# Kernel tuning notes

Hardware: AMD Instinct MI355X
Metric: run time of the kernel (lower is better)

## Reference

```python
import jax, jax.numpy as jnp
import numpy as np
from jax import lax


def ternary_quant(w):
    # Layer-wise ternary quantization: alpha = mean(|w|), threshold = 0.001*alpha
    alpha = lax.stop_gradient(jnp.mean(jnp.abs(w)))
    thr = 0.001 * alpha
    q = jnp.where(w > thr, 1.0, jnp.where(w < -thr, -1.0, 0.0))
    return alpha * q


def setup_inputs() -> dict:
    key = jax.random.key(0)
    k1, k2, k3, k4, k5 = jax.random.split(key, 5)
    B, C, H, W = 32, 384, 64, 64
    fan_in = C * 3 * 3
    bound = 1.0 / np.sqrt(fan_in)  # torch Conv2d default init scale
    return {
        "x": jax.random.normal(k1, (B, C, H, W), dtype=jnp.float32),
        "weight": jax.random.uniform(k2, (C, C, 3, 3), dtype=jnp.float32, minval=-bound, maxval=bound),
        "bias": jax.random.uniform(k3, (C,), dtype=jnp.float32, minval=-bound, maxval=bound),
        "time_emb": jax.random.normal(k4, (B, 512), dtype=jnp.float32),
        "y": jax.random.randint(k5, (B,), 0, 1000, dtype=jnp.int64),
    }


def reference(x, weight, bias, time_emb, y):
    # time_emb and y are accepted but unused, matching Downsample.forward
    qw = ternary_quant(weight)
    out = lax.conv_general_dilated(
        x, qw,
        window_strides=(2, 2),
        padding=((1, 1), (1, 1)),
        dimension_numbers=("NCHW", "OIHW", "NCHW"),
    )
    return out + bias[None, :, None, None]
```

## Files before the change

### kernel.cpp

```cpp
#include <hip/hip_runtime.h>
#include <hip/hip_bf16.h>


#define CIN   384
#define HIN   64
#define WIN   64
#define OHW   32
#define KDIM  3456
#define NWELT 1327104
#define MDIM  32768
#define NT    54

using bf16 = __hip_bfloat16;
typedef __attribute__((ext_vector_type(8))) short short8;
typedef __attribute__((ext_vector_type(4))) float floatx4;
typedef __attribute__((ext_vector_type(2))) unsigned short ushort2v;

#define AS1 __attribute__((address_space(1)))
#define AS3 __attribute__((address_space(3)))
#define DMA16(g, l) __builtin_amdgcn_global_load_lds((const AS1 void*)(g), (AS3 void*)(l), 16, 0, 0)

#define EDGE(N) do { \
    asm volatile("s_waitcnt vmcnt(" #N ")" ::: "memory"); \
    __builtin_amdgcn_s_barrier(); \
    __builtin_amdgcn_sched_barrier(0); \
} while (0)

#define NPART  62
#define ZG_F   16
#define XN_OFF 256
#define WQ_OFF (256 + 100663296)

__global__ void absum_part(const float* __restrict__ w, float* __restrict__ ws) {
    const float4* w4 = (const float4*)w;
    float s = 0.f;
    for (int i = blockIdx.x * 256 + threadIdx.x; i < NWELT / 4; i += NPART * 256) {
        float4 v = w4[i];
        s += fabsf(v.x) + fabsf(v.y) + fabsf(v.z) + fabsf(v.w);
    }
    for (int off = 32; off; off >>= 1) s += __shfl_down(s, off, 64);
    __shared__ float red[4];
    if ((threadIdx.x & 63) == 0) red[threadIdx.x >> 6] = s;
    __syncthreads();
    if (threadIdx.x == 0) ws[2 + blockIdx.x] = red[0] + red[1] + red[2] + red[3];
}

__global__ void absum_final(float* __restrict__ ws) {
    if (threadIdx.x == 0) {
        float s = 0.f;
        for (int i = 0; i < NPART; ++i) s += ws[2 + i];
        float alpha = s * (1.0f / NWELT);
        ws[0] = alpha;
        ws[1] = 1e-3f * alpha;
        ws[ZG_F + 0] = 0.f; ws[ZG_F + 1] = 0.f;
        ws[ZG_F + 2] = 0.f; ws[ZG_F + 3] = 0.f;
    }
}

__global__ void quant_kernel(const float* __restrict__ w, const float* __restrict__ ws,
                             bf16* __restrict__ wq) {
    int j = blockIdx.x * 256 + threadIdx.x;
    if (j >= NWELT) return;
    float thr = ws[1];
    int o = j / KDIM;
    int rmd = j - o * KDIM;
    int khkw = rmd / 384;
    int c = rmd - khkw * 384;
    float v = w[((o * 384 + c) * 9) + khkw];
    float q = (v > thr) ? 1.f : ((v < -thr) ? -1.f : 0.f);
    wq[j] = __float2bfloat16(q);
}

__global__ void nhwc_kernel(const float* __restrict__ x, bf16* __restrict__ xn) {
    int nh = blockIdx.x;
    int n = nh >> 6, h = nh & 63;
    int c0 = blockIdx.y * 64;
    __shared__ bf16 tile[64][66];
    const float* src = x + ((n * CIN + c0) * HIN + h) * WIN;
    for (int i = 0; i < 4; ++i) {
        int s = threadIdx.x + i * 256;
        int cl = s >> 4, w4 = (s & 15) * 4;
        float4 v = *(const float4*)(src + cl * 4096 + w4);
        bf16 t0[2], t1[2];
        t0[0] = __float2bfloat16(v.x); t0[1] = __float2bfloat16(v.y);
        t1[0] = __float2bfloat16(v.z); t1[1] = __float2bfloat16(v.w);
        *(ushort2v*)&tile[cl][w4]     = *(ushort2v*)t0;
        *(ushort2v*)&tile[cl][w4 + 2] = *(ushort2v*)t1;
    }
    __syncthreads();
    bf16* dst = xn + ((size_t)(n * HIN + h) * WIN) * CIN + c0;
    for (int i = 0; i < 2; ++i) {
        int q = threadIdx.x + i * 256;
        int wc = q >> 3, c8 = (q & 7) * 8;
        bf16 tmp[8];
        #pragma unroll
        for (int j = 0; j < 8; ++j) tmp[j] = tile[c8 + j][wc];
        *(short8*)(dst + (size_t)wc * CIN + c8) = *(short8*)tmp;
    }
}

#define BM  128

__global__ __launch_bounds__(512, 2) void conv_gemm(const bf16* __restrict__ xn,
                                                    const bf16* __restrict__ wq,
                                                    const float* __restrict__ ws,
                                                    const float* __restrict__ bias,
                                                    float* __restrict__ out,
                                                    const bf16* __restrict__ zg) {
    __shared__ __align__(16) bf16 lW[2][384 * 64];
    __shared__ __align__(16) bf16 lX[2][128 * 64];
    const int m_base = blockIdx.x * BM;
    const int tid = threadIdx.x;
    const int lane = tid & 63;
    const int wv = tid >> 6;
    const int io = wv & 3;
    const int im = wv >> 2;
    const int g = (lane & 7) ^ (lane >> 3);

    const bf16* pw[2][3];
    int wLoff[2][3];
    #pragma unroll
    for (int h = 0; h < 2; ++h)
        #pragma unroll
        for (int j = 0; j < 3; ++j) {
            int rr = h * 192 + wv * 24 + j * 8;
            pw[h][j] = wq + (size_t)(rr + (lane >> 3)) * KDIM + g * 8;
            wLoff[h][j] = rr * 64;
        }
    const bf16* pxn[2];
    int oh2[2], ow2[2], xLoff[2];
    #pragma unroll
    for (int h = 0; h < 2; ++h) {
        int rr = h * 64 + wv * 8;
        int m = m_base + rr + (lane >> 3);
        int n = m >> 10, oh = (m >> 5) & 31, ow = m & 31;
        pxn[h] = xn + (size_t)n * (HIN * WIN * CIN) + g * 8;
        oh2[h] = 2 * oh - 1;
        ow2[h] = 2 * ow - 1;
        xLoff[h] = rr * 64;
    }

    const int l15 = lane & 15, quad = lane >> 4, l7 = lane & 7;
    const int octA = (quad ^ l7) * 8;
    const int octB = ((4 + quad) ^ l7) * 8;
    int aoff[2][3], boff[2][2];
    #pragma unroll
    for (int h = 0; h < 2; ++h)
        #pragma unroll
        for (int fo = 0; fo < 3; ++fo)
            aoff[h][fo] = (h * 192 + io * 48 + fo * 16 + l15) * 64;
    #pragma unroll
    for (int h = 0; h < 2; ++h)
        #pragma unroll
        for (int fm = 0; fm < 2; ++fm)
            boff[h][fm] = (h * 64 + im * 32 + fm * 16 + l15) * 64;

    floatx4 acc[6][4];
    #pragma unroll
    for (int i = 0; i < 6; ++i)
        #pragma unroll
        for (int j = 0; j < 4; ++j)
            acc[i][j] = (floatx4){0.f, 0.f, 0.f, 0.f};

    {
        #pragma unroll
        for (int j = 0; j < 3; ++j) DMA16(pw[0][j], &lW[0][wLoff[0][j]]);
        {
            int ih = oh2[0], iw = ow2[0];
            const bf16* p = (ih >= 0 && iw >= 0) ? pxn[0] + (ih * WIN + iw) * CIN : zg;
            DMA16(p, &lX[0][xLoff[0]]);
        }
        {
            int ih = oh2[1], iw = ow2[1];
            const bf16* p = (ih >= 0 && iw >= 0) ? pxn[1] + (ih * WIN + iw) * CIN : zg;
            DMA16(p, &lX[0][xLoff[1]]);
        }
        #pragma unroll
        for (int j = 0; j < 3; ++j) DMA16(pw[1][j], &lW[0][wLoff[1][j]]);
        EDGE(4);
    }

    short8 af[2][3], bfl[2][2], bfh[2][2];

    for (int t = 0; t < NT - 1; ++t) {
        bf16* lWc = lW[t & 1];
        bf16* lXc = lX[t & 1];
        bf16* lWn = lW[(t & 1) ^ 1];
        bf16* lXn = lX[(t & 1) ^ 1];
        const int s = t + 1;
        const int kk = s / 6, cs = s - kk * 6;
        const int kh = kk / 3, kw = kk - kh * 3;
        const int ws64 = s * 64;
        const bf16* pxs[2];
        #pragma unroll
        for (int h = 0; h < 2; ++h) {
            int ih = oh2[h] + kh, iw = ow2[h] + kw;
            pxs[h] = (ih >= 0 && iw >= 0) ? pxn[h] + (ih * WIN + iw) * CIN + cs * 64 : zg;
        }

        #pragma unroll
        for (int fo = 0; fo < 3; ++fo) {
            af[0][fo] = *(const short8*)(lWc + aoff[0][fo] + octA);
            af[1][fo] = *(const short8*)(lWc + aoff[0][fo] + octB);
        }
        #pragma unroll
        for (int fm = 0; fm < 2; ++fm) {
            bfl[0][fm] = *(const short8*)(lXc + boff[0][fm] + octA);
            bfl[1][fm] = *(const short8*)(lXc + boff[0][fm] + octB);
        }
        #pragma unroll
        for (int j = 0; j < 3; ++j) DMA16(pw[0][j] + ws64, lWn + wLoff[0][j]);
        EDGE(6);
        __builtin_amdgcn_s_setprio(1);
        #pragma unroll
        for (int ks = 0; ks < 2; ++ks)
            #pragma unroll
            for (int fo = 0; fo < 3; ++fo)
                #pragma unroll
                for (int fm = 0; fm < 2; ++fm)
                    acc[fo][fm] = __builtin_amdgcn_mfma_f32_16x16x32_bf16(
                        af[ks][fo], bfl[ks][fm], acc[fo][fm], 0, 0, 0);
        __builtin_amdgcn_s_setprio(0);

        #pragma unroll
        for (int fm = 0; fm < 2; ++fm) {
            bfh[0][fm] = *(const short8*)(lXc + boff[1][fm] + octA);
            bfh[1][fm] = *(const short8*)(lXc + boff[1][fm] + octB);
        }
        DMA16(pxs[0], lXn + xLoff[0]);
        EDGE(4);
        __builtin_amdgcn_s_setprio(1);
        #pragma unroll
        for (int ks = 0; ks < 2; ++ks)
            #pragma unroll
            for (int fo = 0; fo < 3; ++fo)
                #pragma unroll
                for (int fm = 0; fm < 2; ++fm)
                    acc[fo][2 + fm] = __builtin_amdgcn_mfma_f32_16x16x32_bf16(
                        af[ks][fo], bfh[ks][fm], acc[fo][2 + fm], 0, 0, 0);
        __builtin_amdgcn_s_setprio(0);

        #pragma unroll
        for (int fo = 0; fo < 3; ++fo) {
            af[0][fo] = *(const short8*)(lWc + aoff[1][fo] + octA);
            af[1][fo] = *(const short8*)(lWc + aoff[1][fo] + octB);
        }
        DMA16(pxs[1], lXn + xLoff[1]);
        __builtin_amdgcn_s_setprio(1);
        #pragma unroll
        for (int ks = 0; ks < 2; ++ks)
            #pragma unroll
            for (int fo = 0; fo < 3; ++fo)
                #pragma unroll
                for (int fm = 0; fm < 2; ++fm)
                    acc[3 + fo][2 + fm] = __builtin_amdgcn_mfma_f32_16x16x32_bf16(
                        af[ks][fo], bfh[ks][fm], acc[3 + fo][2 + fm], 0, 0, 0);
        __builtin_amdgcn_s_setprio(0);

        #pragma unroll
        for (int j = 0; j < 3; ++j) DMA16(pw[1][j] + ws64, lWn + wLoff[1][j]);
        EDGE(4);
        __builtin_amdgcn_s_setprio(1);
        #pragma unroll
        for (int ks = 0; ks < 2; ++ks)
            #pragma unroll
            for (int fo = 0; fo < 3; ++fo)
                #pragma unroll
                for (int fm = 0; fm < 2; ++fm)
                    acc[3 + fo][fm] = __builtin_amdgcn_mfma_f32_16x16x32_bf16(
                        af[ks][fo], bfl[ks][fm], acc[3 + fo][fm], 0, 0, 0);
        __builtin_amdgcn_s_setprio(0);
    }

    {
        bf16* lWc = lW[1];
        bf16* lXc = lX[1];
        #pragma unroll
        for (int fo = 0; fo < 3; ++fo) {
            af[0][fo] = *(const short8*)(lWc + aoff[0][fo] + octA);
            af[1][fo] = *(const short8*)(lWc + aoff[0][fo] + octB);
        }
        #pragma unroll
        for (int fm = 0; fm < 2; ++fm) {
            bfl[0][fm] = *(const short8*)(lXc + boff[0][fm] + octA);
            bfl[1][fm] = *(const short8*)(lXc + boff[0][fm] + octB);
        }
        EDGE(3);
        __builtin_amdgcn_s_setprio(1);
        #pragma unroll
        for (int ks = 0; ks < 2; ++ks)
            #pragma unroll
            for (int fo = 0; fo < 3; ++fo)
                #pragma unroll
                for (int fm = 0; fm < 2; ++fm)
                    acc[fo][fm] = __builtin_amdgcn_mfma_f32_16x16x32_bf16(
                        af[ks][fo], bfl[ks][fm], acc[fo][fm], 0, 0, 0);
        __builtin_amdgcn_s_setprio(0);
        #pragma unroll
        for (int fm = 0; fm < 2; ++fm) {
            bfh[0][fm] = *(const short8*)(lXc + boff[1][fm] + octA);
            bfh[1][fm] = *(const short8*)(lXc + boff[1][fm] + octB);
        }
        EDGE(0);
        __builtin_amdgcn_s_setprio(1);
        #pragma unroll
        for (int ks = 0; ks < 2; ++ks)
            #pragma unroll
            for (int fo = 0; fo < 3; ++fo)
                #pragma unroll
                for (int fm = 0; fm < 2; ++fm)
                    acc[fo][2 + fm] = __builtin_amdgcn_mfma_f32_16x16x32_bf16(
                        af[ks][fo], bfh[ks][fm], acc[fo][2 + fm], 0, 0, 0);
        __builtin_amdgcn_s_setprio(0);
        #pragma unroll
        for (int fo = 0; fo < 3; ++fo) {
            af[0][fo] = *(const short8*)(lWc + aoff[1][fo] + octA);
            af[1][fo] = *(const short8*)(lWc + aoff[1][fo] + octB);
        }
        __builtin_amdgcn_s_setprio(1);
        #pragma unroll
        for (int ks = 0; ks < 2; ++ks)
            #pragma unroll
            for (int fo = 0; fo < 3; ++fo)
                #pragma unroll
                for (int fm = 0; fm < 2; ++fm)
                    acc[3 + fo][2 + fm] = __builtin_amdgcn_mfma_f32_16x16x32_bf16(
                        af[ks][fo], bfh[ks][fm], acc[3 + fo][2 + fm], 0, 0, 0);
        __builtin_amdgcn_s_setprio(0);
        __builtin_amdgcn_s_setprio(1);
        #pragma unroll
        for (int ks = 0; ks < 2; ++ks)
            #pragma unroll
            for (int fo = 0; fo < 3; ++fo)
                #pragma unroll
                for (int fm = 0; fm < 2; ++fm)
                    acc[3 + fo][fm] = __builtin_amdgcn_mfma_f32_16x16x32_bf16(
                        af[ks][fo], bfl[ks][fm], acc[3 + fo][fm], 0, 0, 0);
        __builtin_amdgcn_s_setprio(0);
    }

    float alpha = ws[0];
    #pragma unroll
    for (int i = 0; i < 6; ++i) {
        int o0 = (i / 3) * 192 + io * 48 + (i % 3) * 16 + quad * 4;
        #pragma unroll
        for (int j = 0; j < 4; ++j) {
            int m = m_base + (j >> 1) * 64 + im * 32 + (j & 1) * 16 + l15;
            int n = m >> 10, ohh = (m >> 5) & 31, oww = m & 31;
            #pragma unroll
            for (int r = 0; r < 4; ++r) {
                int o = o0 + r;
                out[((n * 384 + o) * OHW + ohh) * OHW + oww] = alpha * acc[i][j][r] + bias[o];
            }
        }
    }
}

extern "C" void kernel_launch(void* const* d_in, const int* in_sizes, int n_in,
                              void* d_out, int out_size, void* d_ws, size_t ws_size,
                              hipStream_t stream) {
    (void)in_sizes; (void)n_in; (void)out_size; (void)ws_size;
    const float* x    = (const float*)d_in[0];
    const float* w    = (const float*)d_in[1];
    const float* bias = (const float*)d_in[2];
    float* out = (float*)d_out;
    float* wsf = (float*)d_ws;
    bf16* xn = (bf16*)((char*)d_ws + XN_OFF);
    bf16* wq = (bf16*)((char*)d_ws + WQ_OFF);
    const bf16* zg = (const bf16*)(wsf + ZG_F);

    absum_part<<<NPART, 256, 0, stream>>>(w, wsf);
    absum_final<<<1, 64, 0, stream>>>(wsf);
    quant_kernel<<<(NWELT + 255) / 256, 256, 0, stream>>>(w, wsf, wq);
    nhwc_kernel<<<dim3(2048, 6), 256, 0, stream>>>(x, xn);
    conv_gemm<<<dim3(MDIM / BM, 1), 512, 0, stream>>>(xn, wq, wsf, bias, out, zg);
}
```

Measured before the change: 426.3 us.

## Fuse NCHW-to-NHWC bf16 conversion into the conv GEMM's input tile loading

```diff
diff --git a/kernel.cpp b/kernel.cpp
--- a/kernel.cpp
+++ b/kernel.cpp
@@ -14,21 +14,25 @@
 using bf16 = __hip_bfloat16;
 typedef __attribute__((ext_vector_type(8))) short short8;
 typedef __attribute__((ext_vector_type(4))) float floatx4;
-typedef __attribute__((ext_vector_type(2))) unsigned short ushort2v;
 
 #define AS1 __attribute__((address_space(1)))
 #define AS3 __attribute__((address_space(3)))
 #define DMA16(g, l) __builtin_amdgcn_global_load_lds((const AS1 void*)(g), (AS3 void*)(l), 16, 0, 0)
 
-#define EDGE(N) do { \
+#define EDGE_V(N) do { \
     asm volatile("s_waitcnt vmcnt(" #N ")" ::: "memory"); \
     __builtin_amdgcn_s_barrier(); \
     __builtin_amdgcn_sched_barrier(0); \
 } while (0)
+#define EDGE_VL(N) do { \
+    asm volatile("s_waitcnt vmcnt(" #N ")" ::: "memory"); \
+    asm volatile("s_waitcnt lgkmcnt(0)" ::: "memory"); \
+    __builtin_amdgcn_s_barrier(); \
+    __builtin_amdgcn_sched_barrier(0); \
+} while (0)
 
 #define NPART  62
 #define ZG_F   16
-#define XN_OFF 256
 #define WQ_OFF (256 + 100663296)
 
 __global__ void absum_part(const float* __restrict__ w, float* __restrict__ ws) {
@@ -71,42 +75,19 @@
     wq[j] = __float2bfloat16(q);
 }
 
-__global__ void nhwc_kernel(const float* __restrict__ x, bf16* __restrict__ xn) {
-    int nh = blockIdx.x;
-    int n = nh >> 6, h = nh & 63;
-    int c0 = blockIdx.y * 64;
-    __shared__ bf16 tile[64][66];
-    const float* src = x + ((n * CIN + c0) * HIN + h) * WIN;
-    for (int i = 0; i < 4; ++i) {
-        int s = threadIdx.x + i * 256;
-        int cl = s >> 4, w4 = (s & 15) * 4;
-        float4 v = *(const float4*)(src + cl * 4096 + w4);
-        bf16 t0[2], t1[2];
-        t0[0] = __float2bfloat16(v.x); t0[1] = __float2bfloat16(v.y);
-        t1[0] = __float2bfloat16(v.z); t1[1] = __float2bfloat16(v.w);
-        *(ushort2v*)&tile[cl][w4]     = *(ushort2v*)t0;
-        *(ushort2v*)&tile[cl][w4 + 2] = *(ushort2v*)t1;
-    }
-    __syncthreads();
-    bf16* dst = xn + ((size_t)(n * HIN + h) * WIN) * CIN + c0;
-    for (int i = 0; i < 2; ++i) {
-        int q = threadIdx.x + i * 256;
-        int wc = q >> 3, c8 = (q & 7) * 8;
-        bf16 tmp[8];
-        #pragma unroll
-        for (int j = 0; j < 8; ++j) tmp[j] = tile[c8 + j][wc];
-        *(short8*)(dst + (size_t)wc * CIN + c8) = *(short8*)tmp;
-    }
-}
-
 #define BM  128
 
-__global__ __launch_bounds__(512, 2) void conv_gemm(const bf16* __restrict__ xn,
+#define CVT(f) ((short)__builtin_bit_cast(unsigned short, __float2bfloat16(f)))
+
+__device__ __forceinline__ void xput(bf16* lXn, int m, int co, short8 v) {
+    *(short8*)((char*)lXn + m * 128 + ((co ^ (m & 7)) << 4)) = v;
+}
+
+__global__ __launch_bounds__(512, 2) void conv_gemm(const float* __restrict__ x,
                                                     const bf16* __restrict__ wq,
                                                     const float* __restrict__ ws,
                                                     const float* __restrict__ bias,
-                                                    float* __restrict__ out,
-                                                    const bf16* __restrict__ zg) {
+                                                    float* __restrict__ out) {
     __shared__ __align__(16) bf16 lW[2][384 * 64];
     __shared__ __align__(16) bf16 lX[2][128 * 64];
     const int m_base = blockIdx.x * BM;
@@ -117,6 +98,9 @@
     const int im = wv >> 2;
     const int g = (lane & 7) ^ (lane >> 3);
 
+    const int n = m_base >> 10;
+    const int oh0 = (m_base >> 5) & 31;
+
     const bf16* pw[2][3];
     int wLoff[2][3];
     #pragma unroll
@@ -127,18 +111,12 @@
             pw[h][j] = wq + (size_t)(rr + (lane >> 3)) * KDIM + g * 8;
             wLoff[h][j] = rr * 64;
         }
-    const bf16* pxn[2];
-    int oh2[2], ow2[2], xLoff[2];
-    #pragma unroll
-    for (int h = 0; h < 2; ++h) {
-        int rr = h * 64 + wv * 8;
-        int m = m_base + rr + (lane >> 3);
-        int n = m >> 10, oh = (m >> 5) & 31, ow = m & 31;
-        pxn[h] = xn + (size_t)n * (HIN * WIN * CIN) + g * 8;
-        oh2[h] = 2 * oh - 1;
-        ow2[h] = 2 * ow - 1;
-        xLoff[h] = rr * 64;
-    }
+
+    const int co  = tid & 7;
+    const int owp = (tid >> 3) & 15;
+    const int ohx = tid >> 7;
+    const int ohb = 2 * (oh0 + ohx) - 1;
+    const float* xrow0 = x + ((size_t)(n * CIN + co * 8) * HIN) * WIN + owp * 4;
 
     const int l15 = lane & 15, quad = lane >> 4, l7 = lane & 7;
     const int octA = (quad ^ l7) * 8;
@@ -162,22 +140,37 @@
         for (int j = 0; j < 4; ++j)
             acc[i][j] = (floatx4){0.f, 0.f, 0.f, 0.f};
 
+    short8 zv;
+    #pragma unroll
+    for (int i = 0; i < 8; ++i) zv[i] = 0;
+
     {
+        float4 xr[8];
+        const int ihv = ohb;
+        if (ihv >= 0) {
+            const float* xb = xrow0 + (size_t)ihv * WIN;
+            #pragma unroll
+            for (int i = 0; i < 8; ++i) xr[i] = *(const float4*)(xb + i * 4096);
+        } else {
+            #pragma unroll
+            for (int i = 0; i < 8; ++i) xr[i] = make_float4(0.f, 0.f, 0.f, 0.f);
+        }
         #pragma unroll
         for (int j = 0; j < 3; ++j) DMA16(pw[0][j], &lW[0][wLoff[0][j]]);
-        {
-            int ih = oh2[0], iw = ow2[0];
-            const bf16* p = (ih >= 0 && iw >= 0) ? pxn[0] + (ih * WIN + iw) * CIN : zg;
-            DMA16(p, &lX[0][xLoff[0]]);
-        }
-        {
-            int ih = oh2[1], iw = ow2[1];
-            const bf16* p = (ih >= 0 && iw >= 0) ? pxn[1] + (ih * WIN + iw) * CIN : zg;
-            DMA16(p, &lX[0][xLoff[1]]);
-        }
         #pragma unroll
         for (int j = 0; j < 3; ++j) DMA16(pw[1][j], &lW[0][wLoff[1][j]]);
-        EDGE(4);
+        short8 v0, v1;
+        if (ihv >= 0) {
+            #pragma unroll
+            for (int i = 0; i < 8; ++i) { v0[i] = CVT(xr[i].y); v1[i] = CVT(xr[i].w); }
+        } else { v0 = zv; v1 = zv; }
+        xput(lX[0], ohx * 32 + owp * 2 + 1, co, v0);
+        if (owp < 15) xput(lX[0], ohx * 32 + owp * 2 + 2, co, v1);
+        if (owp == 0) xput(lX[0], ohx * 32, co, zv);
+        asm volatile("s_waitcnt lgkmcnt(0)" ::: "memory");
+        asm volatile("s_waitcnt vmcnt(3)" ::: "memory");
+        __builtin_amdgcn_s_barrier();
+        __builtin_amdgcn_sched_barrier(0);
     }
 
     short8 af[2][3], bfl[2][2], bfh[2][2];
@@ -188,15 +181,12 @@
         bf16* lWn = lW[(t & 1) ^ 1];
         bf16* lXn = lX[(t & 1) ^ 1];
         const int s = t + 1;
-        const int kk = s / 6, cs = s - kk * 6;
-        const int kh = kk / 3, kw = kk - kh * 3;
-        const int ws64 = s * 64;
-        const bf16* pxs[2];
-        #pragma unroll
-        for (int h = 0; h < 2; ++h) {
-            int ih = oh2[h] + kh, iw = ow2[h] + kw;
-            pxs[h] = (ih >= 0 && iw >= 0) ? pxn[h] + (ih * WIN + iw) * CIN + cs * 64 : zg;
-        }
+        const int cc_s = s / 9;
+        const int khkw_s = s - cc_s * 9;
+        const int kh_s = khkw_s / 3;
+        const int kw_s = khkw_s - kh_s * 3;
+        const int koff = khkw_s * 384 + cc_s * 64;
+        const int ihv = ohb + kh_s;
 
         #pragma unroll
         for (int fo = 0; fo < 3; ++fo) {
@@ -208,9 +198,17 @@
             bfl[0][fm] = *(const short8*)(lXc + boff[0][fm] + octA);
             bfl[1][fm] = *(const short8*)(lXc + boff[0][fm] + octB);
         }
-        #pragma unroll
-        for (int j = 0; j < 3; ++j) DMA16(pw[0][j] + ws64, lWn + wLoff[0][j]);
-        EDGE(6);
+        float4 xr[8];
+        if (ihv >= 0) {
+            const float* xb = xrow0 + ((size_t)cc_s * 64 * HIN + ihv) * WIN;
+            #pragma unroll
+            for (int i = 0; i < 8; ++i) xr[i] = *(const float4*)(xb + i * 4096);
+        } else {
+            #pragma unroll
+            for (int i = 0; i < 8; ++i) xr[i] = make_float4(0.f, 0.f, 0.f, 0.f);
+        }
+        #pragma unroll
+        for (int j = 0; j < 3; ++j) DMA16(pw[0][j] + koff, lWn + wLoff[0][j]);
         __builtin_amdgcn_s_setprio(1);
         #pragma unroll
         for (int ks = 0; ks < 2; ++ks)
@@ -227,8 +225,7 @@
             bfh[0][fm] = *(const short8*)(lXc + boff[1][fm] + octA);
             bfh[1][fm] = *(const short8*)(lXc + boff[1][fm] + octB);
         }
-        DMA16(pxs[0], lXn + xLoff[0]);
-        EDGE(4);
+        EDGE_V(11);
         __builtin_amdgcn_s_setprio(1);
         #pragma unroll
         for (int ks = 0; ks < 2; ++ks)
@@ -245,7 +242,6 @@
             af[0][fo] = *(const short8*)(lWc + aoff[1][fo] + octA);
             af[1][fo] = *(const short8*)(lWc + aoff[1][fo] + octB);
         }
-        DMA16(pxs[1], lXn + xLoff[1]);
         __builtin_amdgcn_s_setprio(1);
         #pragma unroll
         for (int ks = 0; ks < 2; ++ks)
@@ -256,10 +252,30 @@
                     acc[3 + fo][2 + fm] = __builtin_amdgcn_mfma_f32_16x16x32_bf16(
                         af[ks][fo], bfh[ks][fm], acc[3 + fo][2 + fm], 0, 0, 0);
         __builtin_amdgcn_s_setprio(0);
-
-        #pragma unroll
-        for (int j = 0; j < 3; ++j) DMA16(pw[1][j] + ws64, lWn + wLoff[1][j]);
-        EDGE(4);
+        {
+            short8 v0, v1;
+            if (ihv >= 0) {
+                if (kw_s == 1) {
+                    #pragma unroll
+                    for (int i = 0; i < 8; ++i) { v0[i] = CVT(xr[i].x); v1[i] = CVT(xr[i].z); }
+                } else {
+                    #pragma unroll
+                    for (int i = 0; i < 8; ++i) { v0[i] = CVT(xr[i].y); v1[i] = CVT(xr[i].w); }
+                }
+            } else { v0 = zv; v1 = zv; }
+            if (kw_s == 0) {
+                xput(lXn, ohx * 32 + owp * 2 + 1, co, v0);
+                if (owp < 15) xput(lXn, ohx * 32 + owp * 2 + 2, co, v1);
+                if (owp == 0) xput(lXn, ohx * 32, co, zv);
+            } else {
+                xput(lXn, ohx * 32 + owp * 2, co, v0);
+                xput(lXn, ohx * 32 + owp * 2 + 1, co, v1);
+            }
+        }
+
+        #pragma unroll
+        for (int j = 0; j < 3; ++j) DMA16(pw[1][j] + koff, lWn + wLoff[1][j]);
+        EDGE_VL(3);
         __builtin_amdgcn_s_setprio(1);
         #pragma unroll
         for (int ks = 0; ks < 2; ++ks)
@@ -285,7 +301,6 @@
             bfl[0][fm] = *(const short8*)(lXc + boff[0][fm] + octA);
             bfl[1][fm] = *(const short8*)(lXc + boff[0][fm] + octB);
         }
-        EDGE(3);
         __builtin_amdgcn_s_setprio(1);
         #pragma unroll
         for (int ks = 0; ks < 2; ++ks)
@@ -301,7 +316,7 @@
             bfh[0][fm] = *(const short8*)(lXc + boff[1][fm] + octA);
             bfh[1][fm] = *(const short8*)(lXc + boff[1][fm] + octB);
         }
-        EDGE(0);
+        EDGE_V(0);
         __builtin_amdgcn_s_setprio(1);
         #pragma unroll
         for (int ks = 0; ks < 2; ++ks)
@@ -346,11 +361,11 @@
         #pragma unroll
         for (int j = 0; j < 4; ++j) {
             int m = m_base + (j >> 1) * 64 + im * 32 + (j & 1) * 16 + l15;
-            int n = m >> 10, ohh = (m >> 5) & 31, oww = m & 31;
+            int nn = m >> 10, ohh = (m >> 5) & 31, oww = m & 31;
             #pragma unroll
             for (int r = 0; r < 4; ++r) {
                 int o = o0 + r;
-                out[((n * 384 + o) * OHW + ohh) * OHW + oww] = alpha * acc[i][j][r] + bias[o];
+                out[((nn * 384 + o) * OHW + ohh) * OHW + oww] = alpha * acc[i][j][r] + bias[o];
             }
         }
     }
@@ -365,13 +380,10 @@
     const float* bias = (const float*)d_in[2];
     float* out = (float*)d_out;
     float* wsf = (float*)d_ws;
-    bf16* xn = (bf16*)((char*)d_ws + XN_OFF);
     bf16* wq = (bf16*)((char*)d_ws + WQ_OFF);
-    const bf16* zg = (const bf16*)(wsf + ZG_F);
 
     absum_part<<<NPART, 256, 0, stream>>>(w, wsf);
     absum_final<<<1, 64, 0, stream>>>(wsf);
     quant_kernel<<<(NWELT + 255) / 256, 256, 0, stream>>>(w, wsf, wq);
-    nhwc_kernel<<<dim3(2048, 6), 256, 0, stream>>>(x, xn);
-    conv_gemm<<<dim3(MDIM / BM, 1), 512, 0, stream>>>(xn, wq, wsf, bias, out, zg);
-}
+    conv_gemm<<<dim3(MDIM / BM, 1), 512, 0, stream>>>(x, wq, wsf, bias, out);
+}
```

After: 436.0 us. 1.02x slower.

## Triple-buffer activation tiles and prefetch two K-steps ahead in conv GEMM

Applied to the files above, without the earlier changes.

```diff
diff --git a/kernel.cpp b/kernel.cpp
--- a/kernel.cpp
+++ b/kernel.cpp
@@ -20,10 +20,29 @@
 #define AS3 __attribute__((address_space(3)))
 #define DMA16(g, l) __builtin_amdgcn_global_load_lds((const AS1 void*)(g), (AS3 void*)(l), 16, 0, 0)
 
-#define EDGE(N) do { \
+#define EDGE_V(N) do { \
     asm volatile("s_waitcnt vmcnt(" #N ")" ::: "memory"); \
     __builtin_amdgcn_s_barrier(); \
     __builtin_amdgcn_sched_barrier(0); \
+} while (0)
+#define EDGE_VL(N) do { \
+    asm volatile("s_waitcnt vmcnt(" #N ")" ::: "memory"); \
+    asm volatile("s_waitcnt lgkmcnt(0)" ::: "memory"); \
+    __builtin_amdgcn_s_barrier(); \
+    __builtin_amdgcn_sched_barrier(0); \
+} while (0)
+
+#define MFMA_Q(ACCR, ACCC, BF) do { \
+    __builtin_amdgcn_s_setprio(1); \
+    _Pragma("unroll") \
+    for (int ks = 0; ks < 2; ++ks) \
+        _Pragma("unroll") \
+        for (int fo = 0; fo < 3; ++fo) \
+            _Pragma("unroll") \
+            for (int fm = 0; fm < 2; ++fm) \
+                acc[(ACCR) + fo][(ACCC) + fm] = __builtin_amdgcn_mfma_f32_16x16x32_bf16( \
+                    af[ks][fo], BF[ks][fm], acc[(ACCR) + fo][(ACCC) + fm], 0, 0, 0); \
+    __builtin_amdgcn_s_setprio(0); \
 } while (0)
 
 #define NPART  62
@@ -108,7 +127,7 @@
                                                     float* __restrict__ out,
                                                     const bf16* __restrict__ zg) {
     __shared__ __align__(16) bf16 lW[2][384 * 64];
-    __shared__ __align__(16) bf16 lX[2][128 * 64];
+    __shared__ __align__(16) bf16 lX[3][128 * 64];
     const int m_base = blockIdx.x * BM;
     const int tid = threadIdx.x;
     const int lane = tid & 63;
@@ -127,6 +146,7 @@
             pw[h][j] = wq + (size_t)(rr + (lane >> 3)) * KDIM + g * 8;
             wLoff[h][j] = rr * 64;
         }
+
     const bf16* pxn[2];
     int oh2[2], ow2[2], xLoff[2];
     #pragma unroll
@@ -164,39 +184,35 @@
 
     {
         #pragma unroll
-        for (int j = 0; j < 3; ++j) DMA16(pw[0][j], &lW[0][wLoff[0][j]]);
-        {
-            int ih = oh2[0], iw = ow2[0];
-            const bf16* p = (ih >= 0 && iw >= 0) ? pxn[0] + (ih * WIN + iw) * CIN : zg;
-            DMA16(p, &lX[0][xLoff[0]]);
-        }
-        {
-            int ih = oh2[1], iw = ow2[1];
-            const bf16* p = (ih >= 0 && iw >= 0) ? pxn[1] + (ih * WIN + iw) * CIN : zg;
-            DMA16(p, &lX[0][xLoff[1]]);
-        }
-        #pragma unroll
-        for (int j = 0; j < 3; ++j) DMA16(pw[1][j], &lW[0][wLoff[1][j]]);
-        EDGE(4);
+        for (int h = 0; h < 2; ++h) {
+            int ih = oh2[h], iw = ow2[h];
+            const bf16* p = (ih >= 0 && iw >= 0) ? pxn[h] + (ih * WIN + iw) * CIN : zg;
+            DMA16(p, &lX[0][xLoff[h]]);
+        }
+        #pragma unroll
+        for (int h = 0; h < 2; ++h)
+            #pragma unroll
+            for (int j = 0; j < 3; ++j) DMA16(pw[h][j], &lW[0][wLoff[h][j]]);
+        #pragma unroll
+        for (int h = 0; h < 2; ++h) {
+            int ih = oh2[h], iw = ow2[h];
+            const bf16* p = (ih >= 0 && iw >= 0) ? pxn[h] + (ih * WIN + iw) * CIN + 64 : zg;
+            DMA16(p, &lX[1][xLoff[h]]);
+        }
+        EDGE_V(2);
     }
 
     short8 af[2][3], bfl[2][2], bfh[2][2];
 
     for (int t = 0; t < NT - 1; ++t) {
         bf16* lWc = lW[t & 1];
-        bf16* lXc = lX[t & 1];
-        bf16* lWn = lW[(t & 1) ^ 1];
-        bf16* lXn = lX[(t & 1) ^ 1];
-        const int s = t + 1;
-        const int kk = s / 6, cs = s - kk * 6;
-        const int kh = kk / 3, kw = kk - kh * 3;
-        const int ws64 = s * 64;
-        const bf16* pxs[2];
-        #pragma unroll
-        for (int h = 0; h < 2; ++h) {
-            int ih = oh2[h] + kh, iw = ow2[h] + kw;
-            pxs[h] = (ih >= 0 && iw >= 0) ? pxn[h] + (ih * WIN + iw) * CIN + cs * 64 : zg;
-        }
+        const int x_cur = t % 3;
+        bf16* lWn = lW[(t + 1) & 1];
+        bf16* lXn2 = lX[(t + 2) % 3];
+        const int kW = (t + 1) * 64;
+        const int s2 = t + 2;
+        const int khkw2 = s2 / 6, cc2 = s2 - khkw2 * 6;
+        const int kh2 = khkw2 / 3, kw2 = khkw2 - kh2 * 3;
 
         #pragma unroll
         for (int fo = 0; fo < 3; ++fo) {
@@ -205,138 +221,68 @@
         }
         #pragma unroll
         for (int fm = 0; fm < 2; ++fm) {
+            bfl[0][fm] = *(const short8*)(lX[x_cur] + boff[0][fm] + octA);
+            bfl[1][fm] = *(const short8*)(lX[x_cur] + boff[0][fm] + octB);
+        }
+        #pragma unroll
+        for (int h = 0; h < 2; ++h)
+            #pragma unroll
+            for (int j = 0; j < 3; ++j) DMA16(pw[h][j] + kW, lWn + wLoff[h][j]);
+        MFMA_Q(0, 0, bfl);
+
+        #pragma unroll
+        for (int fm = 0; fm < 2; ++fm) {
+            bfh[0][fm] = *(const short8*)(lX[x_cur] + boff[1][fm] + octA);
+            bfh[1][fm] = *(const short8*)(lX[x_cur] + boff[1][fm] + octB);
+        }
+        #pragma unroll
+        for (int h = 0; h < 2; ++h) {
+            int ih = oh2[h] + kh2, iw = ow2[h] + kw2;
+            bool valid = (ih >= 0) & (iw >= 0) & (s2 < NT);
+            const bf16* p = valid ? pxn[h] + (ih * WIN + iw) * CIN + cc2 * 64 : zg;
+            DMA16(p, lXn2 + xLoff[h]);
+        }
+        EDGE_V(8);
+        MFMA_Q(0, 2, bfh);
+
+        #pragma unroll
+        for (int fo = 0; fo < 3; ++fo) {
+            af[0][fo] = *(const short8*)(lWc + aoff[1][fo] + octA);
+            af[1][fo] = *(const short8*)(lWc + aoff[1][fo] + octB);
+        }
+        MFMA_Q(3, 2, bfh);
+
+        EDGE_VL(2);
+        MFMA_Q(3, 0, bfl);
+    }
+
+    {
+        bf16* lWc = lW[1];
+        bf16* lXc = lX[53 % 3];
+        #pragma unroll
+        for (int fo = 0; fo < 3; ++fo) {
+            af[0][fo] = *(const short8*)(lWc + aoff[0][fo] + octA);
+            af[1][fo] = *(const short8*)(lWc + aoff[0][fo] + octB);
+        }
+        #pragma unroll
+        for (int fm = 0; fm < 2; ++fm) {
             bfl[0][fm] = *(const short8*)(lXc + boff[0][fm] + octA);
             bfl[1][fm] = *(const short8*)(lXc + boff[0][fm] + octB);
         }
-        #pragma unroll
-        for (int j = 0; j < 3; ++j) DMA16(pw[0][j] + ws64, lWn + wLoff[0][j]);
-        EDGE(6);
-        __builtin_amdgcn_s_setprio(1);
-        #pragma unroll
-        for (int ks = 0; ks < 2; ++ks)
-            #pragma unroll
-            for (int fo = 0; fo < 3; ++fo)
-                #pragma unroll
-                for (int fm = 0; fm < 2; ++fm)
-                    acc[fo][fm] = __builtin_amdgcn_mfma_f32_16x16x32_bf16(
-                        af[ks][fo], bfl[ks][fm], acc[fo][fm], 0, 0, 0);
-        __builtin_amdgcn_s_setprio(0);
-
+        MFMA_Q(0, 0, bfl);
         #pragma unroll
         for (int fm = 0; fm < 2; ++fm) {
             bfh[0][fm] = *(const short8*)(lXc + boff[1][fm] + octA);
             bfh[1][fm] = *(const short8*)(lXc + boff[1][fm] + octB);
         }
-        DMA16(pxs[0], lXn + xLoff[0]);
-        EDGE(4);
-        __builtin_amdgcn_s_setprio(1);
-        #pragma unroll
-        for (int ks = 0; ks < 2; ++ks)
-            #pragma unroll
-            for (int fo = 0; fo < 3; ++fo)
-                #pragma unroll
-                for (int fm = 0; fm < 2; ++fm)
-                    acc[fo][2 + fm] = __builtin_amdgcn_mfma_f32_16x16x32_bf16(
-                        af[ks][fo], bfh[ks][fm], acc[fo][2 + fm], 0, 0, 0);
-        __builtin_amdgcn_s_setprio(0);
-
+        MFMA_Q(0, 2, bfh);
         #pragma unroll
         for (int fo = 0; fo < 3; ++fo) {
             af[0][fo] = *(const short8*)(lWc + aoff[1][fo] + octA);
             af[1][fo] = *(const short8*)(lWc + aoff[1][fo] + octB);
         }
-        DMA16(pxs[1], lXn + xLoff[1]);
-        __builtin_amdgcn_s_setprio(1);
-        #pragma unroll
-        for (int ks = 0; ks < 2; ++ks)
-            #pragma unroll
-            for (int fo = 0; fo < 3; ++fo)
-                #pragma unroll
-                for (int fm = 0; fm < 2; ++fm)
-                    acc[3 + fo][2 + fm] = __builtin_amdgcn_mfma_f32_16x16x32_bf16(
-                        af[ks][fo], bfh[ks][fm], acc[3 + fo][2 + fm], 0, 0, 0);
-        __builtin_amdgcn_s_setprio(0);
-
-        #pragma unroll
-        for (int j = 0; j < 3; ++j) DMA16(pw[1][j] + ws64, lWn + wLoff[1][j]);
-        EDGE(4);
-        __builtin_amdgcn_s_setprio(1);
-        #pragma unroll
-        for (int ks = 0; ks < 2; ++ks)
-            #pragma unroll
-            for (int fo = 0; fo < 3; ++fo)
-                #pragma unroll
-                for (int fm = 0; fm < 2; ++fm)
-                    acc[3 + fo][fm] = __builtin_amdgcn_mfma_f32_16x16x32_bf16(
-                        af[ks][fo], bfl[ks][fm], acc[3 + fo][fm], 0, 0, 0);
-        __builtin_amdgcn_s_setprio(0);
-    }
-
-    {
-        bf16* lWc = lW[1];
-        bf16* lXc = lX[1];
-        #pragma unroll
-        for (int fo = 0; fo < 3; ++fo) {
-            af[0][fo] = *(const short8*)(lWc + aoff[0][fo] + octA);
-            af[1][fo] = *(const short8*)(lWc + aoff[0][fo] + octB);
-        }
-        #pragma unroll
-        for (int fm = 0; fm < 2; ++fm) {
-            bfl[0][fm] = *(const short8*)(lXc + boff[0][fm] + octA);
-            bfl[1][fm] = *(const short8*)(lXc + boff[0][fm] + octB);
-        }
-        EDGE(3);
-        __builtin_amdgcn_s_setprio(1);
-        #pragma unroll
-        for (int ks = 0; ks < 2; ++ks)
-            #pragma unroll
-            for (int fo = 0; fo < 3; ++fo)
-                #pragma unroll
-                for (int fm = 0; fm < 2; ++fm)
-                    acc[fo][fm] = __builtin_amdgcn_mfma_f32_16x16x32_bf16(
-                        af[ks][fo], bfl[ks][fm], acc[fo][fm], 0, 0, 0);
-        __builtin_amdgcn_s_setprio(0);
-        #pragma unroll
-        for (int fm = 0; fm < 2; ++fm) {
-            bfh[0][fm] = *(const short8*)(lXc + boff[1][fm] + octA);
-            bfh[1][fm] = *(const short8*)(lXc + boff[1][fm] + octB);
-        }
-        EDGE(0);
-        __builtin_amdgcn_s_setprio(1);
-        #pragma unroll
-        for (int ks = 0; ks < 2; ++ks)
-            #pragma unroll
-            for (int fo = 0; fo < 3; ++fo)
-                #pragma unroll
-                for (int fm = 0; fm < 2; ++fm)
-                    acc[fo][2 + fm] = __builtin_amdgcn_mfma_f32_16x16x32_bf16(
-                        af[ks][fo], bfh[ks][fm], acc[fo][2 + fm], 0, 0, 0);
-        __builtin_amdgcn_s_setprio(0);
-        #pragma unroll
-        for (int fo = 0; fo < 3; ++fo) {
-            af[0][fo] = *(const short8*)(lWc + aoff[1][fo] + octA);
-            af[1][fo] = *(const short8*)(lWc + aoff[1][fo] + octB);
-        }
-        __builtin_amdgcn_s_setprio(1);
-        #pragma unroll
-        for (int ks = 0; ks < 2; ++ks)
-            #pragma unroll
-            for (int fo = 0; fo < 3; ++fo)
-                #pragma unroll
-                for (int fm = 0; fm < 2; ++fm)
-                    acc[3 + fo][2 + fm] = __builtin_amdgcn_mfma_f32_16x16x32_bf16(
-                        af[ks][fo], bfh[ks][fm], acc[3 + fo][2 + fm], 0, 0, 0);
-        __builtin_amdgcn_s_setprio(0);
-        __builtin_amdgcn_s_setprio(1);
-        #pragma unroll
-        for (int ks = 0; ks < 2; ++ks)
-            #pragma unroll
-            for (int fo = 0; fo < 3; ++fo)
-                #pragma unroll
-                for (int fm = 0; fm < 2; ++fm)
-                    acc[3 + fo][fm] = __builtin_amdgcn_mfma_f32_16x16x32_bf16(
-                        af[ks][fo], bfl[ks][fm], acc[3 + fo][fm], 0, 0, 0);
-        __builtin_amdgcn_s_setprio(0);
+        MFMA_Q(3, 2, bfh);
+        MFMA_Q(3, 0, bfl);
     }
 
     float alpha = ws[0];
@@ -346,11 +292,11 @@
         #pragma unroll
         for (int j = 0; j < 4; ++j) {
             int m = m_base + (j >> 1) * 64 + im * 32 + (j & 1) * 16 + l15;
-            int n = m >> 10, ohh = (m >> 5) & 31, oww = m & 31;
+            int nn = m >> 10, ohh = (m >> 5) & 31, oww = m & 31;
             #pragma unroll
             for (int r = 0; r < 4; ++r) {
                 int o = o0 + r;
-                out[((n * 384 + o) * OHW + ohh) * OHW + oww] = alpha * acc[i][j][r] + bias[o];
+                out[((nn * 384 + o) * OHW + ohh) * OHW + oww] = alpha * acc[i][j][r] + bias[o];
             }
         }
     }
```

Result: slower. 437.5 us (+2.6%).

## Triple-buffer input tiles and prefetch activations two K-steps ahead

Applied to the files above, without the earlier changes.

```diff
diff --git a/kernel.cpp b/kernel.cpp
--- a/kernel.cpp
+++ b/kernel.cpp
@@ -20,7 +20,7 @@
 #define AS3 __attribute__((address_space(3)))
 #define DMA16(g, l) __builtin_amdgcn_global_load_lds((const AS1 void*)(g), (AS3 void*)(l), 16, 0, 0)
 
-#define EDGE(N) do { \
+#define EDGE_V(N) do { \
     asm volatile("s_waitcnt vmcnt(" #N ")" ::: "memory"); \
     __builtin_amdgcn_s_barrier(); \
     __builtin_amdgcn_sched_barrier(0); \
@@ -108,7 +108,7 @@
                                                     float* __restrict__ out,
                                                     const bf16* __restrict__ zg) {
     __shared__ __align__(16) bf16 lW[2][384 * 64];
-    __shared__ __align__(16) bf16 lX[2][128 * 64];
+    __shared__ __align__(16) bf16 lX[3][128 * 64];
     const int m_base = blockIdx.x * BM;
     const int tid = threadIdx.x;
     const int lane = tid & 63;
@@ -164,38 +164,41 @@
 
     {
         #pragma unroll
-        for (int j = 0; j < 3; ++j) DMA16(pw[0][j], &lW[0][wLoff[0][j]]);
-        {
-            int ih = oh2[0], iw = ow2[0];
-            const bf16* p = (ih >= 0 && iw >= 0) ? pxn[0] + (ih * WIN + iw) * CIN : zg;
-            DMA16(p, &lX[0][xLoff[0]]);
-        }
-        {
-            int ih = oh2[1], iw = ow2[1];
-            const bf16* p = (ih >= 0 && iw >= 0) ? pxn[1] + (ih * WIN + iw) * CIN : zg;
-            DMA16(p, &lX[0][xLoff[1]]);
-        }
-        #pragma unroll
-        for (int j = 0; j < 3; ++j) DMA16(pw[1][j], &lW[0][wLoff[1][j]]);
-        EDGE(4);
+        for (int h = 0; h < 2; ++h) {
+            int ih = oh2[h], iw = ow2[h];
+            const bf16* p = (ih >= 0 && iw >= 0) ? pxn[h] + (ih * WIN + iw) * CIN : zg;
+            DMA16(p, &lX[0][xLoff[h]]);
+        }
+        #pragma unroll
+        for (int h = 0; h < 2; ++h)
+            #pragma unroll
+            for (int j = 0; j < 3; ++j) DMA16(pw[h][j], &lW[0][wLoff[h][j]]);
+        #pragma unroll
+        for (int h = 0; h < 2; ++h) {
+            int ih = oh2[h], iw = ow2[h];
+            const bf16* p = (ih >= 0 && iw >= 0) ? pxn[h] + (ih * WIN + iw) * CIN + 64 : zg;
+            DMA16(p, &lX[1][xLoff[h]]);
+        }
+        EDGE_V(2);
     }
 
     short8 af[2][3], bfl[2][2], bfh[2][2];
 
     for (int t = 0; t < NT - 1; ++t) {
-        bf16* lWc = lW[t & 1];
-        bf16* lXc = lX[t & 1];
-        bf16* lWn = lW[(t & 1) ^ 1];
-        bf16* lXn = lX[(t & 1) ^ 1];
-        const int s = t + 1;
-        const int kk = s / 6, cs = s - kk * 6;
-        const int kh = kk / 3, kw = kk - kh * 3;
-        const int ws64 = s * 64;
+        const bf16* lWc = lW[t & 1];
+        const bf16* lXc = lX[t % 3];
+        bf16* lWn = lW[(t + 1) & 1];
+        bf16* lXn2 = lX[(t + 2) % 3];
+        const int kW = (t + 1) * 64;
+        const int s2 = t + 2;
+        const int kk2 = s2 / 6, cs2 = s2 - kk2 * 6;
+        const int kh2 = kk2 / 3, kw2 = kk2 - kh2 * 3;
         const bf16* pxs[2];
         #pragma unroll
         for (int h = 0; h < 2; ++h) {
-            int ih = oh2[h] + kh, iw = ow2[h] + kw;
-            pxs[h] = (ih >= 0 && iw >= 0) ? pxn[h] + (ih * WIN + iw) * CIN + cs * 64 : zg;
+            int ih = oh2[h] + kh2, iw = ow2[h] + kw2;
+            bool valid = (ih >= 0) & (iw >= 0) & (s2 < NT);
+            pxs[h] = valid ? pxn[h] + (ih * WIN + iw) * CIN + cs2 * 64 : zg;
         }
 
         #pragma unroll
@@ -209,8 +212,8 @@
             bfl[1][fm] = *(const short8*)(lXc + boff[0][fm] + octB);
         }
         #pragma unroll
-        for (int j = 0; j < 3; ++j) DMA16(pw[0][j] + ws64, lWn + wLoff[0][j]);
-        EDGE(6);
+        for (int j = 0; j < 3; ++j) DMA16(pw[0][j] + kW, lWn + wLoff[0][j]);
+        EDGE_V(5);
         __builtin_amdgcn_s_setprio(1);
         #pragma unroll
         for (int ks = 0; ks < 2; ++ks)
@@ -227,8 +230,9 @@
             bfh[0][fm] = *(const short8*)(lXc + boff[1][fm] + octA);
             bfh[1][fm] = *(const short8*)(lXc + boff[1][fm] + octB);
         }
-        DMA16(pxs[0], lXn + xLoff[0]);
-        EDGE(4);
+        #pragma unroll
+        for (int j = 0; j < 3; ++j) DMA16(pw[1][j] + kW, lWn + wLoff[1][j]);
+        EDGE_V(8);
         __builtin_amdgcn_s_setprio(1);
         #pragma unroll
         for (int ks = 0; ks < 2; ++ks)
@@ -245,7 +249,8 @@
             af[0][fo] = *(const short8*)(lWc + aoff[1][fo] + octA);
             af[1][fo] = *(const short8*)(lWc + aoff[1][fo] + octB);
         }
-        DMA16(pxs[1], lXn + xLoff[1]);
+        DMA16(pxs[0], lXn2 + xLoff[0]);
+        EDGE_V(9);
         __builtin_amdgcn_s_setprio(1);
         #pragma unroll
         for (int ks = 0; ks < 2; ++ks)
@@ -257,9 +262,8 @@
                         af[ks][fo], bfh[ks][fm], acc[3 + fo][2 + fm], 0, 0, 0);
         __builtin_amdgcn_s_setprio(0);
 
-        #pragma unroll
-        for (int j = 0; j < 3; ++j) DMA16(pw[1][j] + ws64, lWn + wLoff[1][j]);
-        EDGE(4);
+        DMA16(pxs[1], lXn2 + xLoff[1]);
+        EDGE_V(2);
         __builtin_amdgcn_s_setprio(1);
         #pragma unroll
         for (int ks = 0; ks < 2; ++ks)
@@ -273,8 +277,8 @@
     }
 
     {
-        bf16* lWc = lW[1];
-        bf16* lXc = lX[1];
+        const bf16* lWc = lW[1];
+        const bf16* lXc = lX[53 % 3];
         #pragma unroll
         for (int fo = 0; fo < 3; ++fo) {
             af[0][fo] = *(const short8*)(lWc + aoff[0][fo] + octA);
@@ -285,7 +289,6 @@
             bfl[0][fm] = *(const short8*)(lXc + boff[0][fm] + octA);
             bfl[1][fm] = *(const short8*)(lXc + boff[0][fm] + octB);
         }
-        EDGE(3);
         __builtin_amdgcn_s_setprio(1);
         #pragma unroll
         for (int ks = 0; ks < 2; ++ks)
@@ -301,7 +304,6 @@
             bfh[0][fm] = *(const short8*)(lXc + boff[1][fm] + octA);
             bfh[1][fm] = *(const short8*)(lXc + boff[1][fm] + octB);
         }
-        EDGE(0);
         __builtin_amdgcn_s_setprio(1);
         #pragma unroll
         for (int ks = 0; ks < 2; ++ks)
@@ -346,11 +348,11 @@
         #pragma unroll
         for (int j = 0; j < 4; ++j) {
             int m = m_base + (j >> 1) * 64 + im * 32 + (j & 1) * 16 + l15;
-            int n = m >> 10, ohh = (m >> 5) & 31, oww = m & 31;
+            int nn = m >> 10, ohh = (m >> 5) & 31, oww = m & 31;
             #pragma unroll
             for (int r = 0; r < 4; ++r) {
                 int o = o0 + r;
-                out[((n * 384 + o) * OHW + ohh) * OHW + oww] = alpha * acc[i][j][r] + bias[o];
+                out[((nn * 384 + o) * OHW + ohh) * OHW + oww] = alpha * acc[i][j][r] + bias[o];
             }
         }
     }
```

Result: slower. 442.9 us (+3.9%).
